# Kernel optimization log

Measured on AMD Instinct MI355X. Metric: run time of the kernel, lower is better.

The kernel has to match this reference:

```python
import jax, jax.numpy as jnp
import numpy as np

N_NODES = 100000
N_EDGES = 3200000  # avg degree 32
IN_FEATS = 512
N_HIDDEN = 128
N_CLASSES = 64
K = 10  # n_layers of gated APPNP propagation


def setup_inputs() -> dict:
    key = jax.random.key(0)
    ks = jax.random.split(key, 6)
    features = jax.random.normal(ks[0], (N_NODES, IN_FEATS), dtype=jnp.float32)
    W1 = jax.random.normal(ks[1], (IN_FEATS, N_HIDDEN), dtype=jnp.float32) * (1.0 / np.sqrt(IN_FEATS))
    b1 = jnp.zeros((N_HIDDEN,), jnp.float32)
    W2 = jax.random.normal(ks[2], (N_HIDDEN, N_CLASSES), dtype=jnp.float32) * (1.0 / np.sqrt(N_HIDDEN))
    b2 = jnp.zeros((N_CLASSES,), jnp.float32)
    init_weight_y = jax.random.normal(ks[3], (IN_FEATS, N_CLASSES), dtype=jnp.float32) * (1.0 / np.sqrt(IN_FEATS))
    edge_index = jax.random.randint(ks[4], (2, N_EDGES), 0, N_NODES, dtype=jnp.int32)
    return {
        "features": features, "W1": W1, "b1": b1, "W2": W2, "b2": b2,
        "init_weight_y": init_weight_y, "edge_index": edge_index,
    }


def reference(features, W1, b1, W2, b2, init_weight_y, edge_index):
    # Eval-mode forward: feat/edge dropout are identity.
    src, dst = edge_index[0], edge_index[1]
    n = features.shape[0]
    # Symmetric GCN normalization D^{-1/2} A D^{-1/2} from in-degrees.
    deg = jax.ops.segment_sum(jnp.ones(src.shape, features.dtype), dst, num_segments=n)
    norm = jax.lax.rsqrt(jnp.clip(deg, 1.0))
    ew = (norm[src] * norm[dst])[:, None]  # [E,1] edge weights

    def spmm(x):  # A_hat @ x via gather-multiply-scatter
        return jax.ops.segment_sum(x[src] * ew, dst, num_segments=n)

    # feature transform: dropout(identity) -> linear -> relu
    h = jax.nn.relu(features @ W1 + b1)                      # [N,H]
    logits = jax.nn.softmax(features @ init_weight_y, axis=1)  # [N,C]
    # project predictions before propagation (APPNP propagates class scores)
    h0 = h @ W2 + b2                                         # [N,C]

    def step(carry, _):
        hc, lg = carry
        agg_lg = spmm(lg)                                    # neighbor soft labels
        # gate: per-node agreement between own and aggregated soft labels
        z = jax.nn.sigmoid(jnp.sum(lg * agg_lg, axis=1, keepdims=True))  # [N,1]
        h_new = z * spmm(hc) + (1.0 - z) * h0                # gated APPNP hop
        return (h_new, agg_lg), None

    (h_out, _), _ = jax.lax.scan(step, (h0, logits), None, length=K)
    return h_out
```

## Files before the change

kernel.cpp:

```cpp
#include <hip/hip_runtime.h>

typedef __attribute__((ext_vector_type(8))) short bf16x8;
typedef __attribute__((ext_vector_type(4))) short bf16x4;
typedef __attribute__((ext_vector_type(4))) float f32x4;
typedef __attribute__((ext_vector_type(4))) unsigned int u32x4;

__device__ __forceinline__ unsigned short f2bf(float f) {
  unsigned int u = __float_as_uint(f);
  u += 0x7fffu + ((u >> 16) & 1u);
  return (unsigned short)(u >> 16);
}
__device__ __forceinline__ float bflo(unsigned int w) { return __uint_as_float(w << 16); }
__device__ __forceinline__ float bfhi(unsigned int w) { return __uint_as_float(w & 0xffff0000u); }

__device__ __forceinline__ short* ldsp(short* base, int row, int rowbytes, int colshort) {
  int off = row * rowbytes + colshort * 2;
  off ^= ((row & 7) << 4);
  return (short*)((char*)base + off);
}

#define CHUNK 8192
#define NBMAX 512
#define DCAP 96

__global__ __launch_bounds__(256) void k_bhist(const int* __restrict__ ei, int E, int NB,
                                               int* __restrict__ gcnt, int* __restrict__ wghist) {
  __shared__ int h[NBMAX];
  for (int t = threadIdx.x; t < NB; t += 256) h[t] = 0;
  __syncthreads();
  int base = blockIdx.x * CHUNK;
#pragma unroll
  for (int i = 0; i < CHUNK / 256; ++i) {
    int e = base + i * 256 + threadIdx.x;
    if (e < E) atomicAdd(&h[ei[E + e] >> 8], 1);
  }
  __syncthreads();
  for (int t = threadIdx.x; t < NB; t += 256) {
    int c = h[t];
    wghist[blockIdx.x * NBMAX + t] = c;
    if (c) atomicAdd(&gcnt[t], c);
  }
}

__global__ void k_bscan(const int* __restrict__ gcnt, int* __restrict__ bbase,
                        int* __restrict__ gcur, int* __restrict__ offs, int NB, int N) {
  __shared__ int sm[512];
  int t = threadIdx.x;
  int v = (t < NB) ? gcnt[t] : 0;
  sm[t] = v;
  __syncthreads();
  for (int o = 1; o < 512; o <<= 1) {
    int x = (t >= o) ? sm[t - o] : 0;
    __syncthreads();
    sm[t] += x;
    __syncthreads();
  }
  if (t < NB) { int e = sm[t] - v; bbase[t] = e; gcur[t] = e; }
  if (t == 511) { bbase[NB] = sm[511]; offs[N] = sm[511]; }
}

__global__ __launch_bounds__(256) void k_bucket(const int* __restrict__ ei,
                                                const int* __restrict__ wghist,
                                                int* __restrict__ gcur,
                                                int2* __restrict__ bpairs, int E, int NB) {
  __shared__ int lbase[NBMAX];
  __shared__ int lcur[NBMAX];
  for (int t = threadIdx.x; t < NB; t += 256) {
    int c = wghist[blockIdx.x * NBMAX + t];
    lbase[t] = c ? atomicAdd(&gcur[t], c) : 0;
    lcur[t] = 0;
  }
  __syncthreads();
  int base = blockIdx.x * CHUNK;
#pragma unroll
  for (int i = 0; i < CHUNK / 256; ++i) {
    int e = base + i * 256 + threadIdx.x;
    if (e < E) {
      int s = ei[e], d = ei[E + e];
      int b = d >> 8;
      int p = lbase[b] + atomicAdd(&lcur[b], 1);
      bpairs[p] = make_int2(s, d);
    }
  }
}

__global__ __launch_bounds__(256) void k_csr(const int2* __restrict__ bpairs,
                                             const int* __restrict__ bbase,
                                             int* __restrict__ offs, float* __restrict__ nrm,
                                             int* __restrict__ csr_src,
                                             int* __restrict__ gslots, int N) {
  __shared__ int hist[256];
  __shared__ int scan[256];
  __shared__ int cur[256];
  const int t = threadIdx.x;
  const int b = blockIdx.x;
  const int d0 = b << 8;
  const int nn = min(256, N - d0);
  const int base = bbase[b], end = bbase[b + 1];
  hist[t] = 0;
  __syncthreads();
  for (int e = base + t; e < end; e += 256) atomicAdd(&hist[bpairs[e].y - d0], 1);
  __syncthreads();
  int myc = hist[t];
  scan[t] = myc;
  __syncthreads();
  for (int o = 1; o < 256; o <<= 1) {
    int x = (t >= o) ? scan[t - o] : 0;
    __syncthreads();
    scan[t] += x;
    __syncthreads();
  }
  int excl = scan[t] - myc;
  if (t < nn) {
    offs[d0 + t] = base + excl;
    nrm[d0 + t] = rsqrtf(fmaxf((float)myc, 1.f));
  }
  if (t < 64) {
    int w0 = hist[4 * t + 0], w1 = hist[4 * t + 1];
    int w2 = hist[4 * t + 2], w3 = hist[4 * t + 3];
    gslots[b * 64 + t] = 4 * max(max(w0, w1), max(w2, w3));
  }
  cur[t] = excl;
  __syncthreads();
  for (int e = base + t; e < end; e += 256) {
    int2 pr = bpairs[e];
    int pos = atomicAdd(&cur[pr.y - d0], 1);
    csr_src[base + pos] = pr.x;
  }
}

__global__ void k_scan1(const int* __restrict__ in, int* __restrict__ out,
                        int* __restrict__ bsum, int n) {
  __shared__ int sm[1024];
  int t = threadIdx.x;
  int gid = blockIdx.x * 1024 + t;
  int v = (gid < n) ? in[gid] : 0;
  sm[t] = v;
  __syncthreads();
  for (int off = 1; off < 1024; off <<= 1) {
    int x = (t >= off) ? sm[t - off] : 0;
    __syncthreads();
    sm[t] += x;
    __syncthreads();
  }
  if (gid < n) out[gid] = sm[t] - v;
  if (t == 1023) bsum[blockIdx.x] = sm[1023];
}

__global__ void k_scan2(int* __restrict__ bsum, int nb) {
  __shared__ int sm[128];
  int t = threadIdx.x;
  int v = (t < nb) ? bsum[t] : 0;
  sm[t] = v;
  __syncthreads();
  for (int o = 1; o < 128; o <<= 1) {
    int x = (t >= o) ? sm[t - o] : 0;
    __syncthreads();
    sm[t] += x;
    __syncthreads();
  }
  if (t < nb) bsum[t] = sm[t] - v;
  if (t == 127) bsum[nb] = sm[127];
}

__global__ void k_scan3(int* __restrict__ out, const int* __restrict__ bsum, int n) {
  int gid = blockIdx.x * 1024 + threadIdx.x;
  if (gid < n) out[gid] += bsum[blockIdx.x];
  if (gid == 0) out[n] = bsum[gridDim.x];
}

__global__ __launch_bounds__(64) void k_ell(
    const int* __restrict__ offs, const int* __restrict__ csr_src,
    const int* __restrict__ gof, unsigned* __restrict__ pidx,
    unsigned int* __restrict__ pkA, unsigned int* __restrict__ pkB, int N) {
  __shared__ int buf[4][DCAP];
  __shared__ int srt[4][DCAP];
  int g = blockIdx.x;
  int t = threadIdx.x;
  if (g == 0) {
    pkA[(size_t)N * 64 + t] = 0;
    pkB[(size_t)N * 64 + t] = 0;
  }
  int base = gof[g];
  int slots = gof[g + 1] - base;
  int o[4], d[4];
#pragma unroll
  for (int s = 0; s < 4; ++s) {
    int nd_ = g * 4 + s;
    o[s] = (nd_ < N) ? offs[nd_] : 0;
    d[s] = (nd_ < N) ? (offs[nd_ + 1] - o[s]) : 0;
  }
  const int ls = t >> 4;
  const int ll = t & 15;
  const int dd = d[ls];
  const bool srtable = (dd <= DCAP);
  if (srtable)
    for (int i = ll; i < dd; i += 16) buf[ls][i] = csr_src[o[ls] + i];
  __syncthreads();
  if (srtable) {
    for (int i = ll; i < dd; i += 16) {
      int key = buf[ls][i];
      int r = 0;
      for (int j = 0; j < dd; ++j) {
        int v = buf[ls][j];
        r += (v < key) || (v == key && j < i);
      }
      srt[ls][r] = key;
    }
  }
  __syncthreads();
  unsigned zoff = (unsigned)N << 8;
  for (int j = t; j < slots; j += 64) {
    int i = j >> 2, s = j & 3;
    unsigned v = zoff;
    if (i < d[s]) v = (unsigned)((d[s] <= DCAP) ? srt[s][i] : csr_src[o[s] + i]) << 8;
    pidx[base + j] = v;
  }
}

__global__ void k_wprep(const float* __restrict__ W1, const float* __restrict__ Wy,
                        unsigned short* __restrict__ Wt) {
  int k = blockIdx.x, j = threadIdx.x;
  float v = (j < 128) ? W1[k * 128 + j] : Wy[k * 64 + (j - 128)];
  Wt[j * 512 + k] = f2bf(v);
}
__global__ void k_wprep2(const float* __restrict__ W2, unsigned short* __restrict__ Wt2) {
  int k = blockIdx.x, j = threadIdx.x;
  Wt2[j * 128 + k] = f2bf(W2[k * 64 + j]);
}

__global__ __launch_bounds__(256) void k_transform(
    const unsigned short* __restrict__ Wt, const unsigned short* __restrict__ Wt2,
    const float* __restrict__ X, const float* __restrict__ b1, const float* __restrict__ b2,
    const float* __restrict__ nrm,
    unsigned int* __restrict__ pk0, unsigned short* __restrict__ h0b, int n)
{
  __shared__ short Xs[128 * 32];
  __shared__ short Ws[192 * 32];
  __shared__ short Hs[128 * 128];
  __shared__ short W2s[64 * 128];

  const int tid = threadIdx.x;
  const int w = tid >> 6;
  const int lane = tid & 63;
  const int c = lane & 15;
  const int g = lane >> 4;
  const int m0 = blockIdx.x * 128;

#pragma unroll
  for (int i = 0; i < 4; ++i) {
    int cc = tid + i * 256;
    int j2 = cc >> 4, k8 = (cc & 15) * 8;
    bf16x8 v = *(const bf16x8*)&Wt2[j2 * 128 + k8];
    *(bf16x8*)ldsp(W2s, j2, 256, k8) = v;
  }

  f32x4 zero4 = {0.f, 0.f, 0.f, 0.f};
  f32x4 acc[2][12];
#pragma unroll
  for (int mi = 0; mi < 2; ++mi)
#pragma unroll
    for (int i = 0; i < 12; ++i) acc[mi][i] = zero4;

  const int xr = tid >> 1;
  const int xc = (tid & 1) * 16;
  const int xrow = m0 + xr;

  for (int kk = 0; kk < 512; kk += 32) {
    float4 f[4];
    if (xrow < n) {
      const float4* p = (const float4*)(X + (size_t)xrow * 512 + kk + xc);
      f[0] = p[0]; f[1] = p[1]; f[2] = p[2]; f[3] = p[3];
    } else {
      float4 z = {0.f, 0.f, 0.f, 0.f};
      f[0] = z; f[1] = z; f[2] = z; f[3] = z;
    }
    bf16x8 lo, hi;
    {
      const float* fp = (const float*)f;
#pragma unroll
      for (int q = 0; q < 8; ++q) { lo[q] = (short)f2bf(fp[q]); hi[q] = (short)f2bf(fp[8 + q]); }
    }
    *(bf16x8*)ldsp(Xs, xr, 64, xc) = lo;
    *(bf16x8*)ldsp(Xs, xr, 64, xc + 8) = hi;
#pragma unroll
    for (int i = 0; i < 3; ++i) {
      int cc = tid + i * 256;
      int j = cc >> 2, k8 = (cc & 3) * 8;
      bf16x8 v = *(const bf16x8*)&Wt[j * 512 + kk + k8];
      *(bf16x8*)ldsp(Ws, j, 64, k8) = v;
    }
    __syncthreads();
    bf16x8 bx0 = *(const bf16x8*)ldsp(Xs, w * 32 + c, 64, g * 8);
    bf16x8 bx1 = *(const bf16x8*)ldsp(Xs, w * 32 + 16 + c, 64, g * 8);
#pragma unroll
    for (int jt = 0; jt < 12; ++jt) {
      bf16x8 aw = *(const bf16x8*)ldsp(Ws, jt * 16 + c, 64, g * 8);
      acc[0][jt] = __builtin_amdgcn_mfma_f32_16x16x32_bf16(aw, bx0, acc[0][jt], 0, 0, 0);
      acc[1][jt] = __builtin_amdgcn_mfma_f32_16x16x32_bf16(aw, bx1, acc[1][jt], 0, 0, 0);
    }
    __syncthreads();
  }

  float lv[2][16];
  float inv_[2];
#pragma unroll
  for (int mi = 0; mi < 2; ++mi) {
    int m = w * 32 + mi * 16 + c;
#pragma unroll
    for (int jt = 0; jt < 8; ++jt) {
      int jb = jt * 16 + g * 4;
      bf16x4 hv;
#pragma unroll
      for (int q = 0; q < 4; ++q) {
        float hvf = fmaxf(acc[mi][jt][q] + b1[jb + q], 0.f);
        hv[q] = (short)f2bf(hvf);
      }
      *(bf16x4*)ldsp(Hs, m, 256, jb) = hv;
    }
    float mx = -3.4e38f;
#pragma unroll
    for (int t = 0; t < 4; ++t)
#pragma unroll
      for (int q = 0; q < 4; ++q) {
        float vv = acc[mi][8 + t][q];
        lv[mi][t * 4 + q] = vv;
        mx = fmaxf(mx, vv);
      }
    mx = fmaxf(mx, __shfl_xor(mx, 16, 64));
    mx = fmaxf(mx, __shfl_xor(mx, 32, 64));
    float sum = 0.f;
#pragma unroll
    for (int i = 0; i < 16; ++i) { lv[mi][i] = __expf(lv[mi][i] - mx); sum += lv[mi][i]; }
    sum += __shfl_xor(sum, 16, 64);
    sum += __shfl_xor(sum, 32, 64);
    inv_[mi] = 1.f / sum;
  }
  __syncthreads();

  f32x4 acc2[2][4];
#pragma unroll
  for (int mi = 0; mi < 2; ++mi)
#pragma unroll
    for (int i = 0; i < 4; ++i) acc2[mi][i] = zero4;
#pragma unroll
  for (int kk2 = 0; kk2 < 4; ++kk2) {
    bf16x8 bh0 = *(const bf16x8*)ldsp(Hs, w * 32 + c, 256, kk2 * 32 + g * 8);
    bf16x8 bh1 = *(const bf16x8*)ldsp(Hs, w * 32 + 16 + c, 256, kk2 * 32 + g * 8);
#pragma unroll
    for (int j2t = 0; j2t < 4; ++j2t) {
      bf16x8 a2 = *(const bf16x8*)ldsp(W2s, j2t * 16 + c, 256, kk2 * 32 + g * 8);
      acc2[0][j2t] = __builtin_amdgcn_mfma_f32_16x16x32_bf16(a2, bh0, acc2[0][j2t], 0, 0, 0);
      acc2[1][j2t] = __builtin_amdgcn_mfma_f32_16x16x32_bf16(a2, bh1, acc2[1][j2t], 0, 0, 0);
    }
  }

#pragma unroll
  for (int mi = 0; mi < 2; ++mi) {
    int m = w * 32 + mi * 16 + c;
    int grow = m0 + m;
    if (grow < n) {
      float nd = nrm[grow];
#pragma unroll
      for (int t = 0; t < 4; ++t) {
        int cb = t * 16 + g * 4;
        u32x4 pkv;
        bf16x4 hb;
#pragma unroll
        for (int q = 0; q < 4; ++q) {
          float lg  = lv[mi][t * 4 + q] * inv_[mi];
          float h0v = acc2[mi][t][q] + b2[cb + q];
          hb[q]  = (short)f2bf(h0v);
          pkv[q] = ((unsigned)f2bf(nd * h0v) << 16) | (unsigned)f2bf(nd * lg);
        }
        *(u32x4*)(pk0 + (size_t)grow * 64 + cb) = pkv;
        *(bf16x4*)(h0b + (size_t)grow * 64 + cb) = hb;
      }
    }
  }
}

__global__ __launch_bounds__(256) void k_prop(
    const int* __restrict__ gof, const unsigned* __restrict__ pidx,
    const unsigned int* __restrict__ pk_in, unsigned int* __restrict__ pk_out,
    const unsigned short* __restrict__ h0b, const float* __restrict__ nrm,
    float* __restrict__ final_out, int n, int ng, int last)
{
  const int lane = threadIdx.x & 63;
  const int g = blockIdx.x * 4 + (threadIdx.x >> 6);
  if (g >= ng) return;
  const int sub = lane >> 4;
  const int cq  = lane & 15;
  const int node = g * 4 + sub;
  const int beg = gof[g];
  const int w = (gof[g + 1] - beg) >> 2;
  const char* pkc = (const char*)pk_in;
  const unsigned* ib = pidx + beg + sub;
  const int coff = cq << 4;

  const int nodeC = (node < n) ? node : 0;
  u32x4 own = *(const u32x4*)(pkc + ((size_t)nodeC << 8) + coff);
  float nd = nrm[nodeC];
  bf16x4 h0v = *(const bf16x4*)(h0b + (size_t)nodeC * 64 + cq * 4);

  float aL[4] = {0.f, 0.f, 0.f, 0.f}, aH[4] = {0.f, 0.f, 0.f, 0.f};
  float bL[4] = {0.f, 0.f, 0.f, 0.f}, bH[4] = {0.f, 0.f, 0.f, 0.f};
  int i = 0;
  for (; i + 4 <= w; i += 4) {
    unsigned r0 = ib[4 * i];
    unsigned r1 = ib[4 * i + 4];
    unsigned r2 = ib[4 * i + 8];
    unsigned r3 = ib[4 * i + 12];
    u32x4 w0 = *(const u32x4*)(pkc + r0 + coff);
    u32x4 w1 = *(const u32x4*)(pkc + r1 + coff);
    u32x4 w2 = *(const u32x4*)(pkc + r2 + coff);
    u32x4 w3 = *(const u32x4*)(pkc + r3 + coff);
#pragma unroll
    for (int q = 0; q < 4; ++q) {
      aL[q] += bflo(w0[q]) + bflo(w2[q]);
      aH[q] += bfhi(w0[q]) + bfhi(w2[q]);
      bL[q] += bflo(w1[q]) + bflo(w3[q]);
      bH[q] += bfhi(w1[q]) + bfhi(w3[q]);
    }
  }
  for (; i < w; ++i) {
    unsigned r0 = ib[4 * i];
    u32x4 w0 = *(const u32x4*)(pkc + r0 + coff);
#pragma unroll
    for (int q = 0; q < 4; ++q) { aL[q] += bflo(w0[q]); aH[q] += bfhi(w0[q]); }
  }
#pragma unroll
  for (int q = 0; q < 4; ++q) { aL[q] += bL[q]; aH[q] += bH[q]; }

  if (node >= n) return;
  float p = 0.f;
#pragma unroll
  for (int q = 0; q < 4; ++q) p += bflo(own[q]) * aL[q];
  p += __shfl_xor(p, 1, 64);
  p += __shfl_xor(p, 2, 64);
  p += __shfl_xor(p, 4, 64);
  p += __shfl_xor(p, 8, 64);
  float z = 1.f / (1.f + __expf(-p));

  if (last) {
    float4 o;
    float* op = &o.x;
#pragma unroll
    for (int q = 0; q < 4; ++q) {
      float h0f = __uint_as_float(((unsigned)(unsigned short)h0v[q]) << 16);
      op[q] = z * nd * aH[q] + (1.f - z) * h0f;
    }
    *(float4*)(final_out + (size_t)node * 64 + cq * 4) = o;
  } else {
    u32x4 pkv;
    float nn2 = nd * nd;
#pragma unroll
    for (int q = 0; q < 4; ++q) {
      float h0f = __uint_as_float(((unsigned)(unsigned short)h0v[q]) << 16);
      float hn = z * nd * aH[q] + (1.f - z) * h0f;
      pkv[q] = ((unsigned)f2bf(nd * hn) << 16) | (unsigned)f2bf(nn2 * aL[q]);
    }
    *(u32x4*)((char*)pk_out + ((size_t)node << 8) + coff) = pkv;
  }
}

extern "C" void kernel_launch(void* const* d_in, const int* in_sizes, int n_in,
                              void* d_out, int out_size, void* d_ws, size_t ws_size,
                              hipStream_t stream) {
  (void)n_in; (void)out_size; (void)ws_size;
  const float* X  = (const float*)d_in[0];
  const float* W1 = (const float*)d_in[1];
  const float* b1 = (const float*)d_in[2];
  const float* W2 = (const float*)d_in[3];
  const float* b2 = (const float*)d_in[4];
  const float* Wy = (const float*)d_in[5];
  const int*   ei = (const int*)d_in[6];
  const int N = in_sizes[0] / 512;
  const int E = in_sizes[6] / 2;
  const int NB = (N + 255) >> 8;
  const int NG = NB * 64;
  const int NWG = (E + CHUNK - 1) / CHUNK;

  char* p = (char*)d_ws;
  auto alloc = [&](size_t bytes) -> char* {
    char* r = p; p += (bytes + 255) & ~(size_t)255; return r;
  };
  int*            gcnt    = (int*)  alloc(NBMAX * 4);
  int*            bbase   = (int*)  alloc((NBMAX + 1) * 4);
  int*            gcur    = (int*)  alloc(NBMAX * 4);
  int*            wghist  = (int*)  alloc((size_t)NWG * NBMAX * 4);
  int*            offs    = (int*)  alloc((size_t)(N + 1) * 4);
  float*          nrm     = (float*)alloc((size_t)N * 4);
  int*            csr_src = (int*)  alloc((size_t)E * 4);
  int*            gslots  = (int*)  alloc((size_t)(NG + 1) * 4);
  int*            gof     = (int*)  alloc((size_t)(NG + 1) * 4);
  int*            sbsum   = (int*)  alloc(1024);
  unsigned*       pidx    = (unsigned*)alloc((size_t)2 * E * 4);
  unsigned short* Wt      = (unsigned short*)alloc(192 * 512 * 2);
  unsigned short* Wt2     = (unsigned short*)alloc(64 * 128 * 2);
  size_t pkbytes = (size_t)(N + 1) * 64 * 4;
  size_t bpbytes = (size_t)E * 8;
  char*           shared0 = alloc(pkbytes > bpbytes ? pkbytes : bpbytes);
  int2*           bpairs  = (int2*)shared0;
  unsigned int*   pkA     = (unsigned int*)shared0;
  unsigned int*   pkB     = (unsigned int*)alloc(pkbytes);
  unsigned short* h0b     = (unsigned short*)alloc((size_t)N * 64 * 2);

  hipMemsetAsync(gcnt, 0, NBMAX * 4, stream);

  k_wprep<<<512, 192, 0, stream>>>(W1, Wy, Wt);
  k_wprep2<<<128, 64, 0, stream>>>(W2, Wt2);
  k_bhist<<<NWG, 256, 0, stream>>>(ei, E, NB, gcnt, wghist);
  k_bscan<<<1, 512, 0, stream>>>(gcnt, bbase, gcur, offs, NB, N);
  k_bucket<<<NWG, 256, 0, stream>>>(ei, wghist, gcur, bpairs, E, NB);
  k_csr<<<NB, 256, 0, stream>>>(bpairs, bbase, offs, nrm, csr_src, gslots, N);
  int nb2 = (NG + 1023) / 1024;
  k_scan1<<<nb2, 1024, 0, stream>>>(gslots, gof, sbsum, NG);
  k_scan2<<<1, 128, 0, stream>>>(sbsum, nb2);
  k_scan3<<<nb2, 1024, 0, stream>>>(gof, sbsum, NG);
  k_ell<<<NG, 64, 0, stream>>>(offs, csr_src, gof, pidx, pkA, pkB, N);
  k_transform<<<(N + 127) / 128, 256, 0, stream>>>(Wt, Wt2, X, b1, b2, nrm, pkA, h0b, N);

  for (int k = 0; k < 10; ++k) {
    const unsigned int* in  = (k & 1) ? pkB : pkA;
    unsigned int*       out = (k & 1) ? pkA : pkB;
    k_prop<<<(NG + 3) / 4, 256, 0, stream>>>(gof, pidx, in, out, h0b, nrm,
                                             (float*)d_out, N, NG, (k == 9) ? 1 : 0);
  }
}
```

Measured before the change: 1.265 ms.

## Store propagated soft labels as custom 8-bit codes in separate array

Splits the packed bf16 (h, logits) per-node rows into a bf16 h array and a separate logit array encoded as a custom 8-bit log-like code with scaling by 64. Each edge gather now reads 8+4 bytes per lane instead of 16, cutting the gather traffic in the memory-bound propagation loop. The 8-bit code has a narrow exponent/mantissa range and clamps, which risks accuracy loss in the gate computation. Decoding adds ALU work per edge.

New measurement: 1.167 ms. 1.08x faster.

```diff
diff --git a/kernel.cpp b/kernel.cpp
--- a/kernel.cpp
+++ b/kernel.cpp
@@ -3,7 +3,6 @@
 typedef __attribute__((ext_vector_type(8))) short bf16x8;
 typedef __attribute__((ext_vector_type(4))) short bf16x4;
 typedef __attribute__((ext_vector_type(4))) float f32x4;
-typedef __attribute__((ext_vector_type(4))) unsigned int u32x4;
 
 __device__ __forceinline__ unsigned short f2bf(float f) {
   unsigned int u = __float_as_uint(f);
@@ -12,6 +11,16 @@
 }
 __device__ __forceinline__ float bflo(unsigned int w) { return __uint_as_float(w << 16); }
 __device__ __forceinline__ float bfhi(unsigned int w) { return __uint_as_float(w & 0xffff0000u); }
+
+__device__ __forceinline__ unsigned e8(float f) {
+  unsigned u = __float_as_uint(f) + (1u << 19);
+  int cd = (int)(u >> 20) - 920;
+  cd = cd < 0 ? 0 : (cd > 255 ? 255 : cd);
+  return (unsigned)cd;
+}
+__device__ __forceinline__ float d8(unsigned code) {
+  return __uint_as_float((code << 20) + (115u << 23));
+}
 
 __device__ __forceinline__ short* ldsp(short* base, int row, int rowbytes, int colshort) {
   int off = row * rowbytes + colshort * 2;
@@ -172,14 +181,15 @@
 __global__ __launch_bounds__(64) void k_ell(
     const int* __restrict__ offs, const int* __restrict__ csr_src,
     const int* __restrict__ gof, unsigned* __restrict__ pidx,
-    unsigned int* __restrict__ pkA, unsigned int* __restrict__ pkB, int N) {
+    unsigned* __restrict__ HA, unsigned* __restrict__ HB,
+    unsigned* __restrict__ LA, unsigned* __restrict__ LB, int N) {
   __shared__ int buf[4][DCAP];
   __shared__ int srt[4][DCAP];
   int g = blockIdx.x;
   int t = threadIdx.x;
   if (g == 0) {
-    pkA[(size_t)N * 64 + t] = 0;
-    pkB[(size_t)N * 64 + t] = 0;
+    if (t < 32) { HA[(size_t)N * 32 + t] = 0; HB[(size_t)N * 32 + t] = 0; }
+    if (t < 16) { LA[(size_t)N * 16 + t] = 0; LB[(size_t)N * 16 + t] = 0; }
   }
   int base = gof[g];
   int slots = gof[g + 1] - base;
@@ -209,11 +219,11 @@
     }
   }
   __syncthreads();
-  unsigned zoff = (unsigned)N << 8;
+  unsigned zoff = (unsigned)N << 6;
   for (int j = t; j < slots; j += 64) {
     int i = j >> 2, s = j & 3;
     unsigned v = zoff;
-    if (i < d[s]) v = (unsigned)((d[s] <= DCAP) ? srt[s][i] : csr_src[o[s] + i]) << 8;
+    if (i < d[s]) v = (unsigned)((d[s] <= DCAP) ? srt[s][i] : csr_src[o[s] + i]) << 6;
     pidx[base + j] = v;
   }
 }
@@ -233,7 +243,8 @@
     const unsigned short* __restrict__ Wt, const unsigned short* __restrict__ Wt2,
     const float* __restrict__ X, const float* __restrict__ b1, const float* __restrict__ b2,
     const float* __restrict__ nrm,
-    unsigned int* __restrict__ pk0, unsigned short* __restrict__ h0b, int n)
+    unsigned* __restrict__ Hrow0, unsigned* __restrict__ Lrow0,
+    unsigned short* __restrict__ h0b, int n)
 {
   __shared__ short Xs[128 * 32];
   __shared__ short Ws[192 * 32];
@@ -364,16 +375,22 @@
 #pragma unroll
       for (int t = 0; t < 4; ++t) {
         int cb = t * 16 + g * 4;
-        u32x4 pkv;
         bf16x4 hb;
+        unsigned short hs[4];
+        unsigned lw = 0;
 #pragma unroll
         for (int q = 0; q < 4; ++q) {
           float lg  = lv[mi][t * 4 + q] * inv_[mi];
           float h0v = acc2[mi][t][q] + b2[cb + q];
           hb[q]  = (short)f2bf(h0v);
-          pkv[q] = ((unsigned)f2bf(nd * h0v) << 16) | (unsigned)f2bf(nd * lg);
+          hs[q]  = f2bf(nd * h0v);
+          lw |= e8(64.f * nd * lg) << (8 * q);
         }
-        *(u32x4*)(pk0 + (size_t)grow * 64 + cb) = pkv;
+        uint2 hw;
+        hw.x = (unsigned)hs[0] | ((unsigned)hs[1] << 16);
+        hw.y = (unsigned)hs[2] | ((unsigned)hs[3] << 16);
+        *(uint2*)((char*)Hrow0 + (size_t)grow * 128 + cb * 2) = hw;
+        *(unsigned*)((char*)Lrow0 + (size_t)grow * 64 + cb) = lw;
         *(bf16x4*)(h0b + (size_t)grow * 64 + cb) = hb;
       }
     }
@@ -382,7 +399,8 @@
 
 __global__ __launch_bounds__(256) void k_prop(
     const int* __restrict__ gof, const unsigned* __restrict__ pidx,
-    const unsigned int* __restrict__ pk_in, unsigned int* __restrict__ pk_out,
+    const unsigned* __restrict__ Hin, const unsigned* __restrict__ Lin,
+    unsigned* __restrict__ Hout, unsigned* __restrict__ Lout,
     const unsigned short* __restrict__ h0b, const float* __restrict__ nrm,
     float* __restrict__ final_out, int n, int ng, int last)
 {
@@ -394,53 +412,61 @@
   const int node = g * 4 + sub;
   const int beg = gof[g];
   const int w = (gof[g + 1] - beg) >> 2;
-  const char* pkc = (const char*)pk_in;
+  const char* Hc = (const char*)Hin;
+  const char* Lc = (const char*)Lin;
   const unsigned* ib = pidx + beg + sub;
-  const int coff = cq << 4;
+  const int hco = cq << 3;
+  const int lco = cq << 2;
 
   const int nodeC = (node < n) ? node : 0;
-  u32x4 own = *(const u32x4*)(pkc + ((size_t)nodeC << 8) + coff);
+  unsigned ownl = *(const unsigned*)(Lc + ((size_t)nodeC << 6) + lco);
   float nd = nrm[nodeC];
   bf16x4 h0v = *(const bf16x4*)(h0b + (size_t)nodeC * 64 + cq * 4);
 
-  float aL[4] = {0.f, 0.f, 0.f, 0.f}, aH[4] = {0.f, 0.f, 0.f, 0.f};
-  float bL[4] = {0.f, 0.f, 0.f, 0.f}, bH[4] = {0.f, 0.f, 0.f, 0.f};
+  float aH[4] = {0.f, 0.f, 0.f, 0.f}, aL[4] = {0.f, 0.f, 0.f, 0.f};
+  float bH[4] = {0.f, 0.f, 0.f, 0.f}, bL[4] = {0.f, 0.f, 0.f, 0.f};
   int i = 0;
   for (; i + 4 <= w; i += 4) {
-    unsigned r0 = ib[4 * i];
-    unsigned r1 = ib[4 * i + 4];
-    unsigned r2 = ib[4 * i + 8];
-    unsigned r3 = ib[4 * i + 12];
-    u32x4 w0 = *(const u32x4*)(pkc + r0 + coff);
-    u32x4 w1 = *(const u32x4*)(pkc + r1 + coff);
-    u32x4 w2 = *(const u32x4*)(pkc + r2 + coff);
-    u32x4 w3 = *(const u32x4*)(pkc + r3 + coff);
+    unsigned x0 = ib[4 * i], x1 = ib[4 * i + 4], x2 = ib[4 * i + 8], x3 = ib[4 * i + 12];
+    uint2 h0_ = *(const uint2*)(Hc + (((size_t)x0 << 1) + hco));
+    uint2 h1_ = *(const uint2*)(Hc + (((size_t)x1 << 1) + hco));
+    uint2 h2_ = *(const uint2*)(Hc + (((size_t)x2 << 1) + hco));
+    uint2 h3_ = *(const uint2*)(Hc + (((size_t)x3 << 1) + hco));
+    unsigned l0 = *(const unsigned*)(Lc + (x0 + lco));
+    unsigned l1 = *(const unsigned*)(Lc + (x1 + lco));
+    unsigned l2 = *(const unsigned*)(Lc + (x2 + lco));
+    unsigned l3 = *(const unsigned*)(Lc + (x3 + lco));
+    aH[0] += bflo(h0_.x) + bflo(h2_.x); aH[1] += bfhi(h0_.x) + bfhi(h2_.x);
+    aH[2] += bflo(h0_.y) + bflo(h2_.y); aH[3] += bfhi(h0_.y) + bfhi(h2_.y);
+    bH[0] += bflo(h1_.x) + bflo(h3_.x); bH[1] += bfhi(h1_.x) + bfhi(h3_.x);
+    bH[2] += bflo(h1_.y) + bflo(h3_.y); bH[3] += bfhi(h1_.y) + bfhi(h3_.y);
 #pragma unroll
     for (int q = 0; q < 4; ++q) {
-      aL[q] += bflo(w0[q]) + bflo(w2[q]);
-      aH[q] += bfhi(w0[q]) + bfhi(w2[q]);
-      bL[q] += bflo(w1[q]) + bflo(w3[q]);
-      bH[q] += bfhi(w1[q]) + bfhi(w3[q]);
+      aL[q] += d8((l0 >> (8 * q)) & 255u) + d8((l2 >> (8 * q)) & 255u);
+      bL[q] += d8((l1 >> (8 * q)) & 255u) + d8((l3 >> (8 * q)) & 255u);
     }
   }
   for (; i < w; ++i) {
-    unsigned r0 = ib[4 * i];
-    u32x4 w0 = *(const u32x4*)(pkc + r0 + coff);
-#pragma unroll
-    for (int q = 0; q < 4; ++q) { aL[q] += bflo(w0[q]); aH[q] += bfhi(w0[q]); }
-  }
-#pragma unroll
-  for (int q = 0; q < 4; ++q) { aL[q] += bL[q]; aH[q] += bH[q]; }
+    unsigned x0 = ib[4 * i];
+    uint2 h0_ = *(const uint2*)(Hc + (((size_t)x0 << 1) + hco));
+    unsigned l0 = *(const unsigned*)(Lc + (x0 + lco));
+    aH[0] += bflo(h0_.x); aH[1] += bfhi(h0_.x);
+    aH[2] += bflo(h0_.y); aH[3] += bfhi(h0_.y);
+#pragma unroll
+    for (int q = 0; q < 4; ++q) aL[q] += d8((l0 >> (8 * q)) & 255u);
+  }
+#pragma unroll
+  for (int q = 0; q < 4; ++q) { aH[q] += bH[q]; aL[q] += bL[q]; }
 
   if (node >= n) return;
   float p = 0.f;
 #pragma unroll
-  for (int q = 0; q < 4; ++q) p += bflo(own[q]) * aL[q];
+  for (int q = 0; q < 4; ++q) p += d8((ownl >> (8 * q)) & 255u) * aL[q];
   p += __shfl_xor(p, 1, 64);
   p += __shfl_xor(p, 2, 64);
   p += __shfl_xor(p, 4, 64);
   p += __shfl_xor(p, 8, 64);
-  float z = 1.f / (1.f + __expf(-p));
+  float z = 1.f / (1.f + __expf(-p * (1.f / 4096.f)));
 
   if (last) {
     float4 o;
@@ -452,15 +478,21 @@
     }
     *(float4*)(final_out + (size_t)node * 64 + cq * 4) = o;
   } else {
-    u32x4 pkv;
     float nn2 = nd * nd;
+    unsigned short hs[4];
+    unsigned lw = 0;
 #pragma unroll
     for (int q = 0; q < 4; ++q) {
       float h0f = __uint_as_float(((unsigned)(unsigned short)h0v[q]) << 16);
       float hn = z * nd * aH[q] + (1.f - z) * h0f;
-      pkv[q] = ((unsigned)f2bf(nd * hn) << 16) | (unsigned)f2bf(nn2 * aL[q]);
-    }
-    *(u32x4*)((char*)pk_out + ((size_t)node << 8) + coff) = pkv;
+      hs[q] = f2bf(nd * hn);
+      lw |= e8(nn2 * aL[q]) << (8 * q);
+    }
+    uint2 hw;
+    hw.x = (unsigned)hs[0] | ((unsigned)hs[1] << 16);
+    hw.y = (unsigned)hs[2] | ((unsigned)hs[3] << 16);
+    *(uint2*)((char*)Hout + (((size_t)node << 7) + hco)) = hw;
+    *(unsigned*)((char*)Lout + (((size_t)node << 6) + lco)) = lw;
   }
 }
 
@@ -498,12 +530,15 @@
   unsigned*       pidx    = (unsigned*)alloc((size_t)2 * E * 4);
   unsigned short* Wt      = (unsigned short*)alloc(192 * 512 * 2);
   unsigned short* Wt2     = (unsigned short*)alloc(64 * 128 * 2);
-  size_t pkbytes = (size_t)(N + 1) * 64 * 4;
+  size_t hbytes = (size_t)(N + 1) * 128;
+  size_t lbytes = (size_t)(N + 1) * 64;
   size_t bpbytes = (size_t)E * 8;
-  char*           shared0 = alloc(pkbytes > bpbytes ? pkbytes : bpbytes);
+  char*           shared0 = alloc(hbytes > bpbytes ? hbytes : bpbytes);
   int2*           bpairs  = (int2*)shared0;
-  unsigned int*   pkA     = (unsigned int*)shared0;
-  unsigned int*   pkB     = (unsigned int*)alloc(pkbytes);
+  unsigned*       HA      = (unsigned*)shared0;
+  unsigned*       HB      = (unsigned*)alloc(hbytes);
+  unsigned*       LA      = (unsigned*)alloc(lbytes);
+  unsigned*       LB      = (unsigned*)alloc(lbytes);
   unsigned short* h0b     = (unsigned short*)alloc((size_t)N * 64 * 2);
 
   hipMemsetAsync(gcnt, 0, NBMAX * 4, stream);
@@ -518,13 +553,15 @@
   k_scan1<<<nb2, 1024, 0, stream>>>(gslots, gof, sbsum, NG);
   k_scan2<<<1, 128, 0, stream>>>(sbsum, nb2);
   k_scan3<<<nb2, 1024, 0, stream>>>(gof, sbsum, NG);
-  k_ell<<<NG, 64, 0, stream>>>(offs, csr_src, gof, pidx, pkA, pkB, N);
-  k_transform<<<(N + 127) / 128, 256, 0, stream>>>(Wt, Wt2, X, b1, b2, nrm, pkA, h0b, N);
+  k_ell<<<NG, 64, 0, stream>>>(offs, csr_src, gof, pidx, HA, HB, LA, LB, N);
+  k_transform<<<(N + 127) / 128, 256, 0, stream>>>(Wt, Wt2, X, b1, b2, nrm, HA, LA, h0b, N);
 
   for (int k = 0; k < 10; ++k) {
-    const unsigned int* in  = (k & 1) ? pkB : pkA;
-    unsigned int*       out = (k & 1) ? pkA : pkB;
-    k_prop<<<(NG + 3) / 4, 256, 0, stream>>>(gof, pidx, in, out, h0b, nrm,
+    const unsigned* Hin = (k & 1) ? HB : HA;
+    unsigned*       Hout = (k & 1) ? HA : HB;
+    const unsigned* Lin = (k & 1) ? LB : LA;
+    unsigned*       Lout = (k & 1) ? LA : LB;
+    k_prop<<<(NG + 3) / 4, 256, 0, stream>>>(gof, pidx, Hin, Lin, Hout, Lout, h0b, nrm,
                                              (float*)d_out, N, NG, (k == 9) ? 1 : 0);
   }
 }
```
